# Kernel tuning notes

Hardware: AMD Instinct MI355X
Metric: run time of the kernel (lower is better)

## Reference

```python
import jax, jax.numpy as jnp
import numpy as np
from jax import lax

K = 100
NUM_CLASSES = 80
MIN_X = 1; MIN_Y = 1; MAX_X = 4; MAX_Y = 4   # int(base_layer_range/16) for [16,64,16,64]
KEEP = 300
IOU_TH = 0.5
ROI_H = 2 * MAX_Y + 1  # 9
ROI_W = 2 * MAX_X + 1  # 9
MASK_OUT = 36          # 9 -> two stride-2 deconvs -> 36
SCALE = (36.0 - 1.0) / (9.0 - 1.0)
BN_INV = 1.0 / np.sqrt(1.0 + 1e-3)  # BN eval, running mean 0 / var 1, eps=1e-3
SIZES = [(64, 64), (32, 32), (16, 16)]


def bilinear(img, xx, yy):
    # img [..., H, W]; xx, yy same shape S; border-clamped bilinear sample -> [..., *S]
    H, W = img.shape[-2], img.shape[-1]
    xx = jnp.clip(xx, 0.0, W - 1.0)
    yy = jnp.clip(yy, 0.0, H - 1.0)
    x0f = jnp.floor(xx); y0f = jnp.floor(yy)
    wx = xx - x0f; wy = yy - y0f
    x0 = x0f.astype(jnp.int32); y0 = y0f.astype(jnp.int32)
    x1 = jnp.minimum(x0 + 1, W - 1); y1 = jnp.minimum(y0 + 1, H - 1)
    v00 = img[..., y0, x0]; v01 = img[..., y0, x1]
    v10 = img[..., y1, x0]; v11 = img[..., y1, x1]
    return (1 - wy) * ((1 - wx) * v00 + wx * v01) + wy * ((1 - wx) * v10 + wx * v11)


def roi_align(feat, boxes):
    # feat [C,H,W], boxes [N,4] in feat coords -> [N,C,ROI_H,ROI_W] (sampling_ratio=1)
    n = boxes.shape[0]
    x1, y1, x2, y2 = boxes[:, 0], boxes[:, 1], boxes[:, 2], boxes[:, 3]
    jx = (jnp.arange(ROI_W, dtype=jnp.float32) + 0.5) / ROI_W
    jy = (jnp.arange(ROI_H, dtype=jnp.float32) + 0.5) / ROI_H
    gx = x1[:, None] + (x2 - x1)[:, None] * jx  # [N,ROI_W]
    gy = y1[:, None] + (y2 - y1)[:, None] * jy  # [N,ROI_H]
    xx = jnp.broadcast_to(gx[:, None, :], (n, ROI_H, ROI_W))
    yy = jnp.broadcast_to(gy[:, :, None], (n, ROI_H, ROI_W))
    out = bilinear(feat, xx, yy)  # [C,N,ROI_H,ROI_W]
    return jnp.transpose(out, (1, 0, 2, 3))


def crop_resize(masks, boxes):
    # masks [N,h,w], boxes [N,4] -> [N,MASK_OUT,MASK_OUT]
    n = boxes.shape[0]
    t = jnp.arange(MASK_OUT, dtype=jnp.float32) / (MASK_OUT - 1.0)
    x1, y1, x2, y2 = boxes[:, 0], boxes[:, 1], boxes[:, 2], boxes[:, 3]
    gx = x1[:, None] + (x2 - x1)[:, None] * t
    gy = y1[:, None] + (y2 - y1)[:, None] * t
    xx = jnp.broadcast_to(gx[:, None, :], (n, MASK_OUT, MASK_OUT))
    yy = jnp.broadcast_to(gy[:, :, None], (n, MASK_OUT, MASK_OUT))
    return jax.vmap(bilinear)(masks, xx, yy)


def nms_keep(boxes, scores):
    # greedy NMS, faithful to torchvision semantics; returns bool keep flags [N]
    n = boxes.shape[0]
    x1, y1, x2, y2 = boxes[:, 0], boxes[:, 1], boxes[:, 2], boxes[:, 3]
    area = (x2 - x1) * (y2 - y1)
    ix1 = jnp.maximum(x1[:, None], x1[None, :]); iy1 = jnp.maximum(y1[:, None], y1[None, :])
    ix2 = jnp.minimum(x2[:, None], x2[None, :]); iy2 = jnp.minimum(y2[:, None], y2[None, :])
    inter = jnp.clip(ix2 - ix1, 0.0) * jnp.clip(iy2 - iy1, 0.0)
    iou = inter / (area[:, None] + area[None, :] - inter + 1e-9)
    order = jnp.argsort(-scores)  # stable
    def step(carry, idx):
        supp, keep = carry
        k = jnp.logical_not(supp[idx])
        keep = keep.at[idx].set(k)
        supp = jnp.logical_or(supp, jnp.logical_and(k, iou[idx] > IOU_TH))
        return (supp, keep), None
    init = (jnp.zeros((n,), bool), jnp.zeros((n,), bool))
    (_, keep), _ = lax.scan(step, init, order)
    return keep


def _conv(x, w, b, pad):
    y = lax.conv_general_dilated(x, w, (1, 1), [(pad, pad), (pad, pad)],
                                 dimension_numbers=('NCHW', 'OIHW', 'NCHW'))
    return y + b[None, :, None, None]


def _deconv(x, w, b):
    # ConvTranspose2d(k=2, s=2): fractionally-strided conv, doubles spatial size
    y = lax.conv_general_dilated(x, w, (1, 1), [(1, 1), (1, 1)], lhs_dilation=(2, 2),
                                 dimension_numbers=('NCHW', 'OIHW', 'NCHW'))
    return y + b[None, :, None, None]


def _bn(x, g, b):
    return x * (g * BN_INV)[None, :, None, None] + b[None, :, None, None]


def mask_head(x, c1_w, c1_b, mid_w, mid_b, bn_g, bn_b, d1_w, d1_b, d2_w, d2_b, c5_w, c5_b, c6_w, c6_b):
    r = jax.nn.relu
    h = r(_bn(_conv(x, c1_w, c1_b, 1), bn_g[0], bn_b[0]))
    for j in range(3):  # conv2..conv4
        h = r(_bn(_conv(h, mid_w[j], mid_b[j], 1), bn_g[1 + j], bn_b[1 + j]))
    h = r(_deconv(h, d1_w, d1_b))
    h = r(_bn(_conv(h, c5_w, c5_b, 1), bn_g[4], bn_b[4]))
    h = r(_deconv(h, d2_w, d2_b))
    return jax.nn.sigmoid(_conv(h, c6_w, c6_b, 0))


def _decode_layer(heat, tlr, brr, i, H0, W0):
    C, H, W = heat.shape
    hw = H * W
    scores, inds = lax.top_k(heat.reshape(-1), K)
    clses = (inds // hw).astype(jnp.float32)
    rem = inds % hw
    ys = (rem // W).astype(jnp.float32)
    xs = (rem % W).astype(jnp.float32)
    t = tlr.reshape(2, hw)[:, rem]  # [2,K]
    b = brr.reshape(2, hw)[:, rem]
    rx = float(MAX_X - MIN_X); ry = float(MAX_Y - MIN_Y)
    cx = (MAX_X + MIN_X) / 2.0;  cy = (MAX_Y + MIN_Y) / 2.0
    tlx = jnp.clip(xs - (rx * t[0] + cx), 0.0, float(W))
    tly = jnp.clip(ys - (ry * t[1] + cy), 0.0, float(H))
    brx = jnp.clip(xs + (rx * b[0] + cx), 0.0, float(W))
    bry = jnp.clip(ys + (ry * b[1] + cy), 0.0, float(H))
    boxes = jnp.stack([tlx, tly, brx, bry], 1)
    sc = jnp.where((brx < tlx) | (bry < tly), -1.0, scores)
    mb = jnp.stack([xs - MAX_X, ys - MAX_Y, xs + MAX_X, ys + MAX_Y,
                    jnp.full((K,), float(i))], 1)
    s2, order = lax.top_k(sc, K)  # num_dets(1000) >= K -> full sort by score
    boxes = boxes[order]; mb = mb[order]; cls = clses[order]
    lay = jnp.full((K,), float(i))
    cols = jnp.stack([s2, s2, lay, cls], 1)
    bws = jnp.concatenate([boxes, cols], 1)  # boxes_without_scaling [K,8]
    scale = jnp.array([W0 / W, H0 / H, W0 / W, H0 / H], jnp.float32)
    dets = jnp.concatenate([boxes * scale, cols], 1)
    return dets, bws, mb


def _decode_one(h0, h1, h2, t0, t1, t2, b0, b1, b2, f0, f1, f2,
                c1_w, c1_b, mid_w, mid_b, bn_g, bn_b, d1_w, d1_b, d2_w, d2_b,
                c5_w, c5_b, c6_w, c6_b):
    heats = (h0, h1, h2); tls = (t0, t1, t2); brs = (b0, b1, b2); feats = (f0, f1, f2)
    H0, W0 = heats[0].shape[1], heats[0].shape[2]
    dets_l, bws_l, mb_l = [], [], []
    for i in range(3):
        d, bw, mb = _decode_layer(heats[i], tls[i], brs[i], i, H0, W0)
        dets_l.append(d); bws_l.append(bw); mb_l.append(mb)
    dets = jnp.concatenate(dets_l, 0)   # [300,8]
    bws = jnp.concatenate(bws_l, 0)
    mb = jnp.concatenate(mb_l, 0)       # [300,5]
    # NMS faithful to source: boxes = detections[:,1:5], scores = detections[:,4]
    keep = nms_keep(dets[:, 1:5], dets[:, 4])
    sel = jnp.argsort(-jnp.where(keep, dets[:, 4], -1e9))[:KEEP]
    dets = dets[sel]; bws = bws[sel]; mb = mb[sel]
    # sort by mask layer index descending (features processed last->first)
    ord2 = jnp.argsort(-mb[:, 4])
    dets = dets[ord2]; bws = bws[ord2]; mb = mb[ord2]
    # ROI pool each box from its own layer's feature map
    pooled = jnp.stack([roi_align(feats[i], mb[:, :4]) for i in range(3)], 0)  # [3,N,C,9,9]
    lay = jnp.clip(mb[:, 4].astype(jnp.int32), 0, 2)
    rois = pooled[lay, jnp.arange(KEEP)]  # [N,256,9,9]
    masks_all = mask_head(rois, c1_w, c1_b, mid_w, mid_b, bn_g, bn_b,
                          d1_w, d1_b, d2_w, d2_b, c5_w, c5_b, c6_w, c6_b)  # [N,80,36,36]
    cls = jnp.clip(dets[:, 7].astype(jnp.int32), 0, NUM_CLASSES - 1)
    masks = masks_all[jnp.arange(KEEP), cls]  # [N,36,36] (one-hot scatter/select)
    bws4 = bws[:, :4] - jnp.tile(mb[:, :2], (1, 2))
    norm_boxes = SCALE * bws4
    masks = crop_resize(masks, norm_boxes)
    return dets, masks


def setup_inputs():
    key = jax.random.key(0)
    ks = jax.random.split(key, 32)
    B = 1
    inp = {}
    for i, (H, W) in enumerate(SIZES):
        inp['heat%d' % i] = jax.random.uniform(ks[i], (B, NUM_CLASSES, H, W), jnp.float32)
        inp['tl%d' % i] = 0.1 * jax.random.normal(ks[3 + i], (B, 2, H, W), jnp.float32)
        inp['br%d' % i] = 0.1 * jax.random.normal(ks[6 + i], (B, 2, H, W), jnp.float32)
        inp['feat%d' % i] = jax.random.normal(ks[9 + i], (B, 256, H, W), jnp.float32)
    inp['c1_w'] = 0.05 * jax.random.normal(ks[12], (256, 256, 3, 3), jnp.float32)
    inp['c1_b'] = jnp.zeros((256,), jnp.float32)
    inp['mid_w'] = 0.05 * jax.random.normal(ks[13], (3, 256, 256, 3, 3), jnp.float32)
    inp['mid_b'] = jnp.zeros((3, 256), jnp.float32)
    inp['bn_g'] = jnp.ones((5, 256), jnp.float32)
    inp['bn_b'] = jnp.zeros((5, 256), jnp.float32)
    inp['d1_w'] = 0.05 * jax.random.normal(ks[14], (256, 256, 2, 2), jnp.float32)
    inp['d1_b'] = jnp.zeros((256,), jnp.float32)
    inp['d2_w'] = 0.05 * jax.random.normal(ks[15], (256, 256, 2, 2), jnp.float32)
    inp['d2_b'] = jnp.zeros((256,), jnp.float32)
    inp['c5_w'] = 0.05 * jax.random.normal(ks[16], (256, 256, 3, 3), jnp.float32)
    inp['c5_b'] = jnp.zeros((256,), jnp.float32)
    inp['c6_w'] = 0.05 * jax.random.normal(ks[17], (NUM_CLASSES, 256, 1, 1), jnp.float32)
    inp['c6_b'] = jnp.zeros((NUM_CLASSES,), jnp.float32)
    return inp


def reference(heat0, heat1, heat2, tl0, tl1, tl2, br0, br1, br2, feat0, feat1, feat2,
              c1_w, c1_b, mid_w, mid_b, bn_g, bn_b, d1_w, d1_b, d2_w, d2_b,
              c5_w, c5_b, c6_w, c6_b):
    dets, masks = jax.vmap(_decode_one, in_axes=(0,) * 12 + (None,) * 14)(
        heat0, heat1, heat2, tl0, tl1, tl2, br0, br1, br2, feat0, feat1, feat2,
        c1_w, c1_b, mid_w, mid_b, bn_g, bn_b, d1_w, d1_b, d2_w, d2_b, c5_w, c5_b, c6_w, c6_b)
    return dets, masks  # [B,300,8], [B,300,36,36]
```

## Files before the change

### kernel.cpp

```cpp
#include <hip/hip_runtime.h>
#include <math.h>

typedef __attribute__((ext_vector_type(8))) short bf16x8;
typedef __attribute__((ext_vector_type(4))) float f32x4;

__device__ __forceinline__ unsigned fkey_u(float v){
  unsigned b = __float_as_uint(v);
  return (b & 0x80000000u) ? ~b : (b | 0x80000000u);
}
__device__ __forceinline__ float fkey_inv(unsigned m){
  unsigned b = (m & 0x80000000u) ? (m & 0x7fffffffu) : ~m;
  return __uint_as_float(b);
}
__device__ __forceinline__ unsigned short f2bf(float f){
  unsigned u = __float_as_uint(f);
  unsigned r = (u + 0x7fffu + ((u>>16)&1u)) >> 16;
  return (unsigned short)r;
}
__device__ __forceinline__ unsigned long long shfl_xor_u64(unsigned long long v, int mask){
  int lo = __shfl_xor((int)(unsigned)(v & 0xFFFFFFFFull), mask, 64);
  int hi = __shfl_xor((int)(unsigned)(v >> 32), mask, 64);
  return ((unsigned long long)(unsigned)hi << 32) | (unsigned long long)(unsigned)lo;
}
#define BNI 0.9995003746877732f

template<int E, int J>
__device__ __forceinline__ void reg_step(unsigned long long* key, int t, int k2){
  #pragma unroll
  for (int r=0;r<E;r++){
    if ((r & J)==0){
      int e = t*E + r;
      bool desc = ((e & k2)==0);
      unsigned long long a=key[r], b=key[r^J];
      if (desc ? (a<b) : (a>b)){ key[r]=b; key[r^J]=a; }
    }
  }
}
template<int E>
__device__ __forceinline__ void reg_tail(unsigned long long* key, int t, int k2, int jstart){
  if constexpr (E>=8) { if (jstart>=4) reg_step<E,4>(key,t,k2); }
  if constexpr (E>=4) { if (jstart>=2) reg_step<E,2>(key,t,k2); }
  if (jstart>=1) reg_step<E,1>(key,t,k2);
}
template<int E>
__device__ void bitonic_desc(unsigned long long* key, unsigned long long* lds){
  const int t = threadIdx.x;
  const int N = E*256;
  for (int k2=2;k2<=N;k2<<=1){
    for (int j=k2>>1; j>=E; j>>=1){
      int w = j/E;
      bool lower = ((t & w)==0);
      bool desc  = (((t*E) & k2)==0);
      bool keep_max = (desc == lower);
      if (w < 64){
        #pragma unroll
        for (int r=0;r<E;r++){
          unsigned long long mine=key[r];
          unsigned long long o=shfl_xor_u64(mine, w);
          bool gt = mine > o;
          key[r] = keep_max ? (gt?mine:o) : (gt?o:mine);
        }
      } else {
        __syncthreads();
        #pragma unroll
        for (int r=0;r<E;r++) lds[t*E+r]=key[r];
        __syncthreads();
        #pragma unroll
        for (int r=0;r<E;r++){
          unsigned long long mine=key[r];
          unsigned long long o=lds[(t*E+r)^j];
          bool gt = mine > o;
          key[r] = keep_max ? (gt?mine:o) : (gt?o:mine);
        }
      }
// ... 59 lines not shown
  float Wf = (float)W;
  const float* tl = (layer==0)?tl0:((layer==1)?tl1:tl2);
  const float* br = (layer==0)?br0:((layer==1)?br1:br2);
  int base = (layer==0)?0:((layer==1)?1600:2000);
  int cnt  = (layer==0)?1600:((layer==1)?400:100);
  __shared__ unsigned long long lds[2048];
  __shared__ float scl[100];
  unsigned long long key[8];
  int t = threadIdx.x;
  #pragma unroll
  for (int r=0;r<8;r++){
    int i=t*8+r;
    key[r] = (i<cnt)? c2[base+i] : 0ull;
  }
  bitonic_desc<8>(key, lds);
  unsigned long long kwin=0;
  if (t<100) kwin = lds[t];
  float tlx=0,tly=0,brx=0,bry=0,xs=0,ys=0,clsfv=0,scv=0;
  if (t<100){
    unsigned m=(unsigned)(kwin>>32);
    unsigned gidx = 0xFFFFFFFFu - (unsigned)(kwin & 0xFFFFFFFFull);
    float val = fkey_inv(m);
    int cls = (int)(gidx / (unsigned)hw);
    int rem = (int)(gidx % (unsigned)hw);
    int iy = rem / W, ix = rem % W;
    xs = (float)ix; ys = (float)iy; clsfv = (float)cls;
    float t0=tl[rem], t1=tl[hw+rem], b0=br[rem], b1=br[hw+rem];
    tlx = fminf(fmaxf(xs - (3.0f*t0 + 2.5f), 0.0f), Wf);
    tly = fminf(fmaxf(ys - (3.0f*t1 + 2.5f), 0.0f), Wf);
    brx = fminf(fmaxf(xs + (3.0f*b0 + 2.5f), 0.0f), Wf);
    bry = fminf(fmaxf(ys + (3.0f*b1 + 2.5f), 0.0f), Wf);
    scv = ((brx<tlx)||(bry<tly)) ? -1.0f : val;
    scl[t]=scv;
  }
  __syncthreads();
  if (t<100){
    int rank=0;
    for (int i=0;i<100;i++){
      float si=scl[i];
      rank += ((si>scv)||(si==scv && i<t)) ? 1 : 0;
    }
    int row = layer*100 + rank;
    float sx = (float)(1<<layer);
    float* dr = dets + row*8;
    dr[0]=tlx*sx; dr[1]=tly*sx; dr[2]=brx*sx; dr[3]=bry*sx;
    dr[4]=scv; dr[5]=scv; dr[6]=(float)layer; dr[7]=clsfv;
    float* bwr = bws + row*8;
    bwr[0]=tlx;bwr[1]=tly;bwr[2]=brx;bwr[3]=bry;bwr[4]=scv;bwr[5]=scv;bwr[6]=(float)layer;bwr[7]=clsfv;
    float* mr = mbw + row*5;
    mr[0]=xs-4.0f; mr[1]=ys-4.0f; mr[2]=xs+4.0f; mr[3]=ys+4.0f; mr[4]=(float)layer;
  }
}

__global__ __launch_bounds__(512) void k_nms(
    const float* __restrict__ dets, const float* __restrict__ bws, const float* __restrict__ mbw,
    float* __restrict__ out_dets, float* __restrict__ mbf, int* __restrict__ clsf,
    int* __restrict__ layf, float* __restrict__ nbox)
{
  __shared__ float bx1[300],by1[300],bx2[300],by2[300],ar[300],sc[300],ly[300],kk[300],lq[300];
  __shared__ unsigned long long sm[300][5];
  __shared__ int order_[300], keep_[300], sel_[300], fperm[300];
  __shared__ unsigned long long sw[5];
  int t = threadIdx.x;
  if (t<300){
    const float* r = dets + t*8;
    bx1[t]=r[1]; by1[t]=r[2]; bx2[t]=r[3]; by2[t]=r[4];
    sc[t]=r[4];
    ar[t]=(r[3]-r[1])*(r[4]-r[2]);
    ly[t]=mbw[t*5+4];
  }
  __syncthreads();
  if (t<300){
    unsigned long long w[5]={0,0,0,0,0};
    float a=ar[t], X1=bx1[t],Y1=by1[t],X2=bx2[t],Y2=by2[t];
    for (int j=0;j<300;j++){
      float ix1=fmaxf(X1,bx1[j]), iy1=fmaxf(Y1,by1[j]);
      float ix2=fminf(X2,bx2[j]), iy2=fminf(Y2,by2[j]);
      float it = fmaxf(ix2-ix1,0.0f)*fmaxf(iy2-iy1,0.0f);
      float iou = it/(a+ar[j]-it+1e-9f);
      if (iou>0.5f) w[j>>6] |= (1ull<<(j&63));
    }
    #pragma unroll
    for (int q=0;q<5;q++) sm[t][q]=w[q];
    int rank=0; float s=sc[t];
    for (int j=0;j<300;j++){
      float sj=sc[j];
      rank += ((sj>s)||(sj==s&&j<t)) ? 1 : 0;
    }
    order_[rank]=t;
  }
  __syncthreads();
  if (t==0){
    for (int q=0;q<5;q++) sw[q]=0;
    for (int q=0;q<300;q++){
      int idx=order_[q];
      int k = (int)(!((sw[idx>>6]>>(idx&63))&1ull));
      keep_[idx]=k;
      if (k){
        for (int w2=0;w2<5;w2++) sw[w2]|=sm[idx][w2];
      }
    }
  }
  __syncthreads();
  if (t<300) kk[t] = keep_[t] ? sc[t] : -1000000000.0f;
  __syncthreads();
  if (t<300){
    float s=kk[t]; int rank=0;
    for (int j=0;j<300;j++){
      float sj=kk[j];
      rank += ((sj>s)||(sj==s&&j<t)) ? 1 : 0;
    }
    sel_[rank]=t;
  }
  __syncthreads();
  if (t<300) lq[t]=ly[sel_[t]];
  __syncthreads();
  if (t<300){
    float l=lq[t]; int rank=0;
    for (int j=0;j<300;j++){
      float lj=lq[j];
      rank += ((lj>l)||(lj==l&&j<t)) ? 1 : 0;
    }
    fperm[rank]=sel_[t];
  }
  __syncthreads();
  if (t<300){
    int src=fperm[t];
    const float* dr=dets+src*8;
    #pragma unroll
    for (int c=0;c<8;c++) out_dets[t*8+c]=dr[c];
    const float* mr=mbw+src*5;
    #pragma unroll
    for (int c=0;c<5;c++) mbf[t*5+c]=mr[c];
    int cc=(int)dr[7]; cc = cc<0?0:(cc>79?79:cc); clsf[t]=cc;
    int lv=(int)mr[4]; lv = lv<0?0:(lv>2?2:lv); layf[t]=lv;
    const float* bw=bws+src*8;
    nbox[t*4+0]=4.375f*(bw[0]-mr[0]);
    nbox[t*4+1]=4.375f*(bw[1]-mr[1]);
    nbox[t*4+2]=4.375f*(bw[2]-mr[0]);
    nbox[t*4+3]=4.375f*(bw[3]-mr[1]);
  }
}

__global__ __launch_bounds__(256) void k_roi(
    const float* __restrict__ f0,const float* __restrict__ f1,const float* __restrict__ f2,
    const float* __restrict__ mbf, const int* __restrict__ layf,
    unsigned short* __restrict__ rois, int r0)
{
  int nl = blockIdx.x; int g = r0 + nl;
  __shared__ int ix0[9], ix1[9], iy0[9], iy1[9];
  __shared__ float wx[9], wy[9];
  int lay = layf[g];
  int W = 64>>lay;
  float Wf1 = (float)(W-1);
  const float* feat = (lay==0)?f0:((lay==1)?f1:f2);
  int t=threadIdx.x;
  if (t<9){
    float x1=mbf[g*5+0], x2=mbf[g*5+2];
    float jx = ((float)t + 0.5f)/9.0f;
    float gx = x1 + (x2-x1)*jx;
    float xx = fminf(fmaxf(gx,0.0f), Wf1);
    float x0f = floorf(xx);
    wx[t]=xx-x0f;
    int x0=(int)x0f; ix0[t]=x0; ix1[t]=min(x0+1,W-1);
  } else if (t>=16 && t<25){
    int j=t-16;
    float y1=mbf[g*5+1], y2=mbf[g*5+3];
    float jy=((float)j+0.5f)/9.0f;
    float gy=y1+(y2-y1)*jy;
    float yy=fminf(fmaxf(gy,0.0f),Wf1);
    float y0f=floorf(yy);
    wy[j]=yy-y0f;
    int y0=(int)y0f; iy0[j]=y0; iy1[j]=min(y0+1,W-1);
  }
  __syncthreads();
  int c=t;
  const float* fp = feat + (size_t)c*W*W;
  unsigned short* op = rois + (size_t)nl*81*256;
  for (int p=0;p<81;p++){
    int py=p/9, px=p%9;
    float v00=fp[iy0[py]*W+ix0[px]];
    float v01=fp[iy0[py]*W+ix1[px]];
    float v10=fp[iy1[py]*W+ix0[px]];
    float v11=fp[iy1[py]*W+ix1[px]];
    float wxx=wx[px], wyy=wy[py];
    float v = (1.0f-wyy)*((1.0f-wxx)*v00 + wxx*v01) + wyy*((1.0f-wxx)*v10 + wxx*v11);
    op[(size_t)p*256 + c] = f2bf(v);
  }
}

__global__ __launch_bounds__(64) void k_wprep3(
    const float* __restrict__ c1w, const float* __restrict__ midw, const float* __restrict__ c5w,
    unsigned short* __restrict__ WB)
{
  int b = blockIdx.x, c = blockIdx.y, l = threadIdx.x;
  int t = b>>7;
  const float* src = (c==0)? c1w : (c<=3 ? midw + (size_t)(c-1)*589824 : c5w);
  unsigned short* dst = WB + (size_t)c*589824 + ((size_t)b<<9) + l*8;
  int co = (b&15)*16 + (l&15);
  int cib = ((b>>4)&7)*32 + ((l>>4)<<3);
  #pragma unroll
  for (int j=0;j<8;j++) dst[j] = f2bf(src[((size_t)co*256 + cib + j)*9 + t]);
}
__global__ __launch_bounds__(64) void k_wprep2(
    const float* __restrict__ d1w, const float* __restrict__ d2w,
    unsigned short* __restrict__ WD)
{
  int b = blockIdx.x, c = blockIdx.y, l = threadIdx.x;
  int t = b>>7;
  const float* src = (c==0)? d1w : d2w;
  unsigned short* dst = WD + (size_t)c*262144 + ((size_t)b<<9) + l*8;
  int co = (b&15)*16 + (l&15);
  int cib = ((b>>4)&7)*32 + ((l>>4)<<3);
  #pragma unroll
  for (int j=0;j<8;j++) dst[j] = f2bf(src[((size_t)co*256 + cib + j)*4 + t]);
}

__global__ __launch_bounds__(256,2) void k_mconv9(
    const unsigned short* __restrict__ Xg, unsigned short* __restrict__ Yg,
    const unsigned short* __restrict__ WBc,
    const float* __restrict__ Bc, const float* __restrict__ Gg, const float* __restrict__ Bn)
{
  __shared__ __align__(16) unsigned short Xp[121*264];
  int tid=threadIdx.x, l=tid&63, w=tid>>6;
  const unsigned short* Xr = Xg + (size_t)blockIdx.x*81*256;
  for (int idx=tid; idx<121*32; idx+=256){
    int pp=idx>>5, k8=idx&31;
    int py=pp/11-1, px=pp%11-1;
    uint4 v{0,0,0,0};
    if ((unsigned)py<9u && (unsigned)px<9u) v = *(const uint4*)(Xr + ((py*9+px)<<8) + (k8<<3));
    *(uint4*)&Xp[pp*264 + (k8<<3)] = v;
  }
  __syncthreads();
  int pixb[6];
  #pragma unroll
  for (int mt=0;mt<6;mt++){ int m=mt*16+(l&15); if(m>80)m=80; pixb[mt]=(m/9)*11+(m%9); }
  int kg=(l>>4)<<3;
  f32x4 acc[6][4] = {};
  const unsigned short* wbase = WBc + (size_t)l*8;
  for (int t9=0;t9<9;t9++){
    int toff=(t9/3)*11 + (t9%3);
    for (int kc=0;kc<8;kc++){
      bf16x8 a[6], b[4];
      #pragma unroll
      for (int mt=0;mt<6;mt++) a[mt] = *(const bf16x8*)&Xp[(pixb[mt]+toff)*264 + (kc<<5) + kg];
      #pragma unroll
      for (int nn=0;nn<4;nn++) b[nn] = *(const bf16x8*)(wbase + ((size_t)(((t9<<3)+kc)*16 + (w<<2)+nn)<<9));
      #pragma unroll
      for (int mt=0;mt<6;mt++){
        #pragma unroll
        for (int nn=0;nn<4;nn++)
          acc[mt][nn] = __builtin_amdgcn_mfma_f32_16x16x32_bf16(a[mt], b[nn], acc[mt][nn], 0,0,0);
      }
    }
  }
  unsigned short* Yr = Yg + (size_t)blockIdx.x*81*256;
  int rb=(l>>4)<<2;
  #pragma unroll
  for (int nn=0;nn<4;nn++){
    int co=(w<<6)+(nn<<4)+(l&15);
    float bc=Bc[co], gm=Gg[co]*BNI, bb=Bn[co];
    #pragma unroll
    for (int mt=0;mt<6;mt++){
      #pragma unroll
      for (int r=0;r<4;r++){
        int m=mt*16+rb+r;
        if (m<81){
          float v=fmaxf((acc[mt][nn][r]+bc)*gm+bb, 0.f);
          Yr[m*256+co]=f2bf(v);
        }
      }
    }
  }
}

__global__ __launch_bounds__(256,2) void k_mdeconv1(
    const unsigned short* __restrict__ Xg, unsigned short* __restrict__ Yg,
    const unsigned short* __restrict__ WD1, const float* __restrict__ Bd)
{
  __shared__ __align__(16) unsigned short Xp[81*264];
  int tid=threadIdx.x, l=tid&63, w=tid>>6;
  int tp=blockIdx.y;
  const unsigned short* Xr = Xg + (size_t)blockIdx.x*81*256;
  for (int idx=tid; idx<81*32; idx+=256){
    int pp=idx>>5, k8=idx&31;
    *(uint4*)&Xp[pp*264+(k8<<3)] = *(const uint4*)(Xr + (pp<<8)+(k8<<3));
  }
  __syncthreads();
  int pixb[6];
  #pragma unroll
  for (int mt=0;mt<6;mt++){ int m=mt*16+(l&15); pixb[mt]=(m>80)?80:m; }
  int kg=(l>>4)<<3;
  f32x4 acc[6][4] = {};
  const unsigned short* wbase = WD1 + (size_t)tp*65536 + (size_t)l*8;
  for (int kc=0;kc<8;kc++){
    bf16x8 a[6], b[4];
    #pragma unroll
    for (int mt=0;mt<6;mt++) a[mt] = *(const bf16x8*)&Xp[pixb[mt]*264 + (kc<<5) + kg];
    #pragma unroll
    for (int nn=0;nn<4;nn++) b[nn] = *(const bf16x8*)(wbase + ((size_t)(kc*16 + (w<<2)+nn)<<9));
    #pragma unroll
    for (int mt=0;mt<6;mt++){
      #pragma unroll
      for (int nn=0;nn<4;nn++)
        acc[mt][nn] = __builtin_amdgcn_mfma_f32_16x16x32_bf16(a[mt], b[nn], acc[mt][nn], 0,0,0);
    }
  }
  unsigned short* Yr = Yg + (size_t)blockIdx.x*324*256;
  int ky=tp>>1, kx=tp&1;
  int rb=(l>>4)<<2;
  #pragma unroll
  for (int nn=0;nn<4;nn++){
    int co=(w<<6)+(nn<<4)+(l&15);
    float bd=Bd[co];
    #pragma unroll
    for (int mt=0;mt<6;mt++){
      #pragma unroll
      for (int r=0;r<4;r++){
        int m=mt*16+rb+r;
        if (m<81){
          int iy=m/9, ix=m%9;
          int opx=(2*iy+1-ky)*18 + (2*ix+1-kx);
          Yr[opx*256+co]=f2bf(fmaxf(acc[mt][nn][r]+bd,0.f));
        }
      }
    }
  }
}

__global__ __launch_bounds__(256,2) void k_mconv18(
    const unsigned short* __restrict__ Xg, unsigned short* __restrict__ Yg,
    const unsigned short* __restrict__ WBc,
    const float* __restrict__ Bc, const float* __restrict__ Gg, const float* __restrict__ Bn)
{
  __shared__ __align__(16) unsigned short Xp[160*136];
  int tid=threadIdx.x, l=tid&63, w=tid>>6;
  int rg=blockIdx.y;
  const unsigned short* Xr = Xg + (size_t)blockIdx.x*324*256;
  int pixb[7];
  #pragma unroll
  for (int mt=0;mt<7;mt++){ int m=mt*16+(l&15); if(m>107)m=107; pixb[mt]=(m/18)*20+(m%18); }
  int kg=(l>>4)<<3;
  f32x4 acc[7][4] = {};
  const unsigned short* wbase = WBc + (size_t)l*8;
  for (int h=0;h<2;h++){
    __syncthreads();
    for (int idx=tid; idx<160*16; idx+=256){
      int pp=idx>>4, k8=idx&15;
      int py=rg*6-1+pp/20, px=pp%20-1;
      uint4 v{0,0,0,0};
      if ((unsigned)py<18u && (unsigned)px<18u)
        v = *(const uint4*)(Xr + ((py*18+px)<<8) + (h<<7) + (k8<<3));
      *(uint4*)&Xp[pp*136 + (k8<<3)] = v;
    }
    __syncthreads();
    for (int t9=0;t9<9;t9++){
      int toff=(t9/3)*20 + (t9%3);
      for (int kc=0;kc<4;kc++){
        int kcg=(h<<2)+kc;
        bf16x8 a[7], b[4];
        #pragma unroll
        for (int mt=0;mt<7;mt++) a[mt] = *(const bf16x8*)&Xp[(pixb[mt]+toff)*136 + (kc<<5) + kg];
        #pragma unroll
        for (int nn=0;nn<4;nn++) b[nn] = *(const bf16x8*)(wbase + ((size_t)(((t9<<3)+kcg)*16 + (w<<2)+nn)<<9));
        #pragma unroll
        for (int mt=0;mt<7;mt++){
          #pragma unroll
          for (int nn=0;nn<4;nn++)
            acc[mt][nn] = __builtin_amdgcn_mfma_f32_16x16x32_bf16(a[mt], b[nn], acc[mt][nn], 0,0,0);
        }
      }
    }
  }
  unsigned short* Yr = Yg + (size_t)blockIdx.x*324*256;
  int rb=(l>>4)<<2;
  #pragma unroll
  for (int nn=0;nn<4;nn++){
    int co=(w<<6)+(nn<<4)+(l&15);
    float bc=Bc[co], gm=Gg[co]*BNI, bb=Bn[co];
    #pragma unroll
    for (int mt=0;mt<7;mt++){
      #pragma unroll
      for (int r=0;r<4;r++){
        int m=mt*16+rb+r;
        if (m<108){
          int opx=rg*108+m;
          Yr[opx*256+co]=f2bf(fmaxf((acc[mt][nn][r]+bc)*gm+bb, 0.f));
        }
      }
    }
  }
}

__global__ __launch_bounds__(256,2) void k_mdec2c6(
    const unsigned short* __restrict__ Xg,
    const unsigned short* __restrict__ WD2, const float* __restrict__ Bd,
    const float* __restrict__ W6, const float* __restrict__ B6,
    const int* __restrict__ clsf, float* __restrict__ mask36, int r0)
{
  __shared__ __align__(16) unsigned short Xp[108*264];
  __shared__ float part[4][112];
  int tid=threadIdx.x, l=tid&63, w=tid>>6;
  int tp=blockIdx.y, rg=blockIdx.z;
  int g=r0+blockIdx.x;
  const unsigned short* Xr = Xg + (size_t)blockIdx.x*324*256 + (size_t)rg*108*256;
  for (int idx=tid; idx<108*32; idx+=256){
    int pp=idx>>5, k8=idx&31;
    *(uint4*)&Xp[pp*264+(k8<<3)] = *(const uint4*)(Xr + (pp<<8)+(k8<<3));
  }
  __syncthreads();
  int pixb[7];
  #pragma unroll
  for (int mt=0;mt<7;mt++){ int m=mt*16+(l&15); pixb[mt]=(m>107)?107:m; }
  int kg=(l>>4)<<3;
  f32x4 acc[7][4] = {};
  const unsigned short* wbase = WD2 + (size_t)tp*65536 + (size_t)l*8;
  for (int kc=0;kc<8;kc++){
    bf16x8 a[7], b[4];
    #pragma unroll
    for (int mt=0;mt<7;mt++) a[mt] = *(const bf16x8*)&Xp[pixb[mt]*264 + (kc<<5) + kg];
    #pragma unroll
    for (int nn=0;nn<4;nn++) b[nn] = *(const bf16x8*)(wbase + ((size_t)(kc*16 + (w<<2)+nn)<<9));
    #pragma unroll
    for (int mt=0;mt<7;mt++){
      #pragma unroll
      for (int nn=0;nn<4;nn++)
        acc[mt][nn] = __builtin_amdgcn_mfma_f32_16x16x32_bf16(a[mt], b[nn], acc[mt][nn], 0,0,0);
    }
  }
  int cls=clsf[g];
  float w6v[4], bdv[4];
// ... 66 lines not shown
  if (n_in >= 12 && in_sizes[1] == 2*64*64) {
    for (int l=0;l<3;l++){ iH[l]=l*4+0; iT[l]=l*4+1; iB[l]=l*4+2; iF[l]=l*4+3; }
  } else {
    for (int l=0;l<3;l++){ iH[l]=l; iT[l]=3+l; iB[l]=6+l; iF[l]=9+l; }
  }
  const float* heat0=(const float*)d_in[iH[0]];
  const float* heat1=(const float*)d_in[iH[1]];
  const float* heat2=(const float*)d_in[iH[2]];
  const float* tl0=(const float*)d_in[iT[0]];
  const float* tl1=(const float*)d_in[iT[1]];
  const float* tl2=(const float*)d_in[iT[2]];
  const float* br0=(const float*)d_in[iB[0]];
  const float* br1=(const float*)d_in[iB[1]];
  const float* br2=(const float*)d_in[iB[2]];
  const float* feat0=(const float*)d_in[iF[0]];
  const float* feat1=(const float*)d_in[iF[1]];
  const float* feat2=(const float*)d_in[iF[2]];
  const float* c1w=(const float*)d_in[12];
  const float* c1b=(const float*)d_in[13];
  const float* midw=(const float*)d_in[14];
  const float* midb=(const float*)d_in[15];
  const float* bng=(const float*)d_in[16];
  const float* bnb=(const float*)d_in[17];
  const float* d1w=(const float*)d_in[18];
  const float* d1b=(const float*)d_in[19];
  const float* d2w=(const float*)d_in[20];
  const float* d2b=(const float*)d_in[21];
  const float* c5w=(const float*)d_in[22];
  const float* c5b=(const float*)d_in[23];
  const float* c6w=(const float*)d_in[24];
  const float* c6b=(const float*)d_in[25];
  float* out=(float*)d_out;

  char* ws=(char*)d_ws;
  size_t cur=0;
  auto alloc=[&](size_t bytes)->char*{
    char* p=ws+cur;
    cur=(cur+bytes+255)&~(size_t)255;
    return p;
  };
  unsigned short* WB=(unsigned short*)alloc(5ull*589824*2);
  unsigned short* WD=(unsigned short*)alloc(2ull*262144*2);
  unsigned long long* c1s=(unsigned long long*)alloc(420ull*100*8);
  unsigned long long* c2s=(unsigned long long*)alloc(21ull*100*8);
  float* detsw=(float*)alloc(300*8*4);
  float* bwsw=(float*)alloc(300*8*4);
  float* mbw=(float*)alloc(300*5*4);
  float* mbf=(float*)alloc(300*5*4);
  int* clsf=(int*)alloc(300*4);
  int* layf=(int*)alloc(300*4);
  float* nbox=(float*)alloc(300*4*4);
  float* mask36=(float*)alloc(300ull*1296*4);
  size_t fixed=cur;
  size_t perroi = (size_t)(3*81 + 2*324)*256*2;
  size_t avail = (ws_size>fixed+4096)? (ws_size-fixed-4096):0;
  int NRC = (int)(avail/perroi);
  if (NRC>300) NRC=300;
  if (NRC<1) NRC=1;
  unsigned short* X0 =(unsigned short*)alloc((size_t)NRC*81*256*2);
  unsigned short* A9 =(unsigned short*)alloc((size_t)NRC*81*256*2);
  unsigned short* B9 =(unsigned short*)alloc((size_t)NRC*81*256*2);
  unsigned short* C18=(unsigned short*)alloc((size_t)NRC*324*256*2);
  unsigned short* D18=(unsigned short*)alloc((size_t)NRC*324*256*2);

  k_wprep3<<<dim3(1152,5),dim3(64),0,stream>>>(c1w,midw,c5w,WB);
  k_wprep2<<<dim3(512,2),dim3(64),0,stream>>>(d1w,d2w,WD);

  k_sel1<<<dim3(420),dim3(256),0,stream>>>(heat0,heat1,heat2,c1s);
  k_sel2<<<dim3(21),dim3(256),0,stream>>>(c1s,c2s);
  k_sel3_decode<<<dim3(3),dim3(256),0,stream>>>(c2s,tl0,tl1,tl2,br0,br1,br2,detsw,bwsw,mbw);
  k_nms<<<dim3(1),dim3(512),0,stream>>>(detsw,bwsw,mbw,out,mbf,clsf,layf,nbox);

  for (int r0=0;r0<300;r0+=NRC){
    int nr = (300-r0 < NRC)? (300-r0) : NRC;
    k_roi<<<dim3(nr),dim3(256),0,stream>>>(feat0,feat1,feat2,mbf,layf,X0,r0);
    k_mconv9<<<dim3(nr),dim3(256),0,stream>>>(X0,A9,WB,               c1b,       bng,      bnb);
    k_mconv9<<<dim3(nr),dim3(256),0,stream>>>(A9,B9,WB+1ull*589824,   midb,      bng+256,  bnb+256);
    k_mconv9<<<dim3(nr),dim3(256),0,stream>>>(B9,A9,WB+2ull*589824,   midb+256,  bng+512,  bnb+512);
    k_mconv9<<<dim3(nr),dim3(256),0,stream>>>(A9,B9,WB+3ull*589824,   midb+512,  bng+768,  bnb+768);
    k_mdeconv1<<<dim3(nr,4),dim3(256),0,stream>>>(B9,C18,WD,d1b);
    k_mconv18<<<dim3(nr,3),dim3(256),0,stream>>>(C18,D18,WB+4ull*589824, c5b, bng+1024, bnb+1024);
    k_mdec2c6<<<dim3(nr,4,3),dim3(256),0,stream>>>(D18,WD+262144,d2b,c6w,c6b,clsf,mask36,r0);
  }
  k_crop<<<dim3(300),dim3(256),0,stream>>>(mask36,nbox,out+2400);
}
```

Baseline: 693.1 us.

## Fuse ROI align with four 3x3 convs; parallelize NMS; split conv18 output channels

Result: slower. 769.6 us (+11.0%).

```diff
diff --git a/kernel.cpp b/kernel.cpp
--- a/kernel.cpp
+++ b/kernel.cpp
@@ -20,6 +20,11 @@
 __device__ __forceinline__ unsigned long long shfl_xor_u64(unsigned long long v, int mask){
   int lo = __shfl_xor((int)(unsigned)(v & 0xFFFFFFFFull), mask, 64);
   int hi = __shfl_xor((int)(unsigned)(v >> 32), mask, 64);
+  return ((unsigned long long)(unsigned)hi << 32) | (unsigned long long)(unsigned)lo;
+}
+__device__ __forceinline__ unsigned long long bshfl_u64(unsigned long long v, int lane){
+  int lo = __shfl((int)(unsigned)(v & 0xFFFFFFFFull), lane, 64);
+  int hi = __shfl((int)(unsigned)(v >> 32), lane, 64);
   return ((unsigned long long)(unsigned)hi << 32) | (unsigned long long)(unsigned)lo;
 }
 #define BNI 0.9995003746877732f
@@ -185,76 +190,122 @@
   }
 }
 
-__global__ __launch_bounds__(512) void k_nms(
+#define NMS_STEP(P, OC, M) { \
+  int idx=__shfl((OC),(P),64); \
+  unsigned long long supw=bshfl_u64(sup, idx>>6); \
+  int kq=(int)((~(supw>>(idx&63)))&1ull); \
+  if (t==0) keep_[idx]=kq; \
+  unsigned long long v0=bshfl_u64(M[0],(P)); \
+  unsigned long long v1=bshfl_u64(M[1],(P)); \
+  unsigned long long v2=bshfl_u64(M[2],(P)); \
+  unsigned long long v3=bshfl_u64(M[3],(P)); \
+  unsigned long long v4=bshfl_u64(M[4],(P)); \
+  unsigned long long mv=(t==0)?v0:((t==1)?v1:((t==2)?v2:((t==3)?v3:((t==4)?v4:0ull)))); \
+  if (kq) sup|=mv; }
+
+__global__ __launch_bounds__(320) void k_nms(
     const float* __restrict__ dets, const float* __restrict__ bws, const float* __restrict__ mbw,
     float* __restrict__ out_dets, float* __restrict__ mbf, int* __restrict__ clsf,
     int* __restrict__ layf, float* __restrict__ nbox)
 {
-  __shared__ float bx1[300],by1[300],bx2[300],by2[300],ar[300],sc[300],ly[300],kk[300],lq[300];
-  __shared__ unsigned long long sm[300][5];
+  __shared__ __align__(16) float4 bq[300];
+  __shared__ __align__(16) float sc[300];
+  __shared__ __align__(16) float kk[300];
+  __shared__ __align__(16) float lq[300];
+  __shared__ float lyv[300];
+  __shared__ unsigned long long sm_ord[300][5];
   __shared__ int order_[300], keep_[300], sel_[300], fperm[300];
-  __shared__ unsigned long long sw[5];
   int t = threadIdx.x;
+  float X1=0,Y1=0,X2=0,Y2=0,S=0,A=0;
   if (t<300){
     const float* r = dets + t*8;
-    bx1[t]=r[1]; by1[t]=r[2]; bx2[t]=r[3]; by2[t]=r[4];
-    sc[t]=r[4];
-    ar[t]=(r[3]-r[1])*(r[4]-r[2]);
-    ly[t]=mbw[t*5+4];
+    X1=r[1];Y1=r[2];X2=r[3];Y2=r[4];
+    S=r[4];
+    A=(X2-X1)*(Y2-Y1);
+    bq[t]=make_float4(X1,Y1,X2,Y2);
+    sc[t]=S;
+    lyv[t]=mbw[t*5+4];
   }
   __syncthreads();
   if (t<300){
-    unsigned long long w[5]={0,0,0,0,0};
-    float a=ar[t], X1=bx1[t],Y1=by1[t],X2=bx2[t],Y2=by2[t];
-    for (int j=0;j<300;j++){
-      float ix1=fmaxf(X1,bx1[j]), iy1=fmaxf(Y1,by1[j]);
-      float ix2=fminf(X2,bx2[j]), iy2=fminf(Y2,by2[j]);
-      float it = fmaxf(ix2-ix1,0.0f)*fmaxf(iy2-iy1,0.0f);
-      float iou = it/(a+ar[j]-it+1e-9f);
-      if (iou>0.5f) w[j>>6] |= (1ull<<(j&63));
-    }
-    #pragma unroll
-    for (int q=0;q<5;q++) sm[t][q]=w[q];
-    int rank=0; float s=sc[t];
-    for (int j=0;j<300;j++){
-      float sj=sc[j];
-      rank += ((sj>s)||(sj==s&&j<t)) ? 1 : 0;
+    int rank=0;
+    for (int j4=0;j4<75;j4++){
+      float4 s4=*(const float4*)&sc[j4*4];
+      int j=j4*4;
+      rank += ((s4.x>S)||(s4.x==S&&(j+0)<t)) ? 1:0;
+      rank += ((s4.y>S)||(s4.y==S&&(j+1)<t)) ? 1:0;
+      rank += ((s4.z>S)||(s4.z==S&&(j+2)<t)) ? 1:0;
+      rank += ((s4.w>S)||(s4.w==S&&(j+3)<t)) ? 1:0;
+    }
+    unsigned long long wrow[5];
+    #pragma unroll
+    for (int jw=0;jw<5;jw++){
+      unsigned long long bits=0;
+      int lim=(jw==4)?44:64;
+      for (int jj=0;jj<lim;jj++){
+        int j=jw*64+jj;
+        float4 q=bq[j];
+        float aj=(q.z-q.x)*(q.w-q.y);
+        float ix1=fmaxf(X1,q.x), iy1=fmaxf(Y1,q.y);
+        float ix2=fminf(X2,q.z), iy2=fminf(Y2,q.w);
+        float it=fmaxf(ix2-ix1,0.f)*fmaxf(iy2-iy1,0.f);
+        float iou=it/(A+aj-it+1e-9f);
+        bits |= ((unsigned long long)(iou>0.5f))<<jj;
+      }
+      wrow[jw]=bits;
     }
     order_[rank]=t;
-  }
-  __syncthreads();
-  if (t==0){
-    for (int q=0;q<5;q++) sw[q]=0;
-    for (int q=0;q<300;q++){
-      int idx=order_[q];
-      int k = (int)(!((sw[idx>>6]>>(idx&63))&1ull));
-      keep_[idx]=k;
-      if (k){
-        for (int w2=0;w2<5;w2++) sw[w2]|=sm[idx][w2];
-      }
-    }
+    #pragma unroll
+    for (int q=0;q<5;q++) sm_ord[rank][q]=wrow[q];
+  }
+  __syncthreads();
+  if (t<64){
+    int o0=order_[t], o1=order_[64+t], o2=order_[128+t], o3=order_[192+t];
+    int o4=(t<44)? order_[256+t] : 0;
+    unsigned long long m0[5],m1[5],m2[5],m3[5],m4[5];
+    #pragma unroll
+    for (int q=0;q<5;q++){
+      m0[q]=sm_ord[t][q]; m1[q]=sm_ord[64+t][q];
+      m2[q]=sm_ord[128+t][q]; m3[q]=sm_ord[192+t][q];
+      m4[q]=(t<44)? sm_ord[256+t][q] : 0ull;
+    }
+    unsigned long long sup=0;
+    for (int p=0;p<64;p++) NMS_STEP(p,o0,m0);
+    for (int p=0;p<64;p++) NMS_STEP(p,o1,m1);
+    for (int p=0;p<64;p++) NMS_STEP(p,o2,m2);
+    for (int p=0;p<64;p++) NMS_STEP(p,o3,m3);
+    for (int p=0;p<44;p++) NMS_STEP(p,o4,m4);
   }
   __syncthreads();
   if (t<300) kk[t] = keep_[t] ? sc[t] : -1000000000.0f;
   __syncthreads();
+  float KV=0; int rank2=0;
   if (t<300){
-    float s=kk[t]; int rank=0;
-    for (int j=0;j<300;j++){
-      float sj=kk[j];
-      rank += ((sj>s)||(sj==s&&j<t)) ? 1 : 0;
-    }
-    sel_[rank]=t;
-  }
-  __syncthreads();
-  if (t<300) lq[t]=ly[sel_[t]];
+    KV=kk[t];
+    for (int j4=0;j4<75;j4++){
+      float4 s4=*(const float4*)&kk[j4*4];
+      int j=j4*4;
+      rank2 += ((s4.x>KV)||(s4.x==KV&&(j+0)<t)) ? 1:0;
+      rank2 += ((s4.y>KV)||(s4.y==KV&&(j+1)<t)) ? 1:0;
+      rank2 += ((s4.z>KV)||(s4.z==KV&&(j+2)<t)) ? 1:0;
+      rank2 += ((s4.w>KV)||(s4.w==KV&&(j+3)<t)) ? 1:0;
+    }
+    sel_[rank2]=t;
+  }
+  __syncthreads();
+  if (t<300) lq[t]=lyv[sel_[t]];
   __syncthreads();
   if (t<300){
-    float l=lq[t]; int rank=0;
-    for (int j=0;j<300;j++){
-      float lj=lq[j];
-      rank += ((lj>l)||(lj==l&&j<t)) ? 1 : 0;
-    }
-    fperm[rank]=sel_[t];
+    float L=lq[t]; int rank3=0;
+    for (int j4=0;j4<75;j4++){
+      float4 s4=*(const float4*)&lq[j4*4];
+      int j=j4*4;
+      rank3 += ((s4.x>L)||(s4.x==L&&(j+0)<t)) ? 1:0;
+      rank3 += ((s4.y>L)||(s4.y==L&&(j+1)<t)) ? 1:0;
+      rank3 += ((s4.z>L)||(s4.z==L&&(j+2)<t)) ? 1:0;
+      rank3 += ((s4.w>L)||(s4.w==L&&(j+3)<t)) ? 1:0;
+    }
+    fperm[rank3]=sel_[t];
   }
   __syncthreads();
   if (t<300){
@@ -275,53 +326,6 @@
   }
 }
 
-__global__ __launch_bounds__(256) void k_roi(
-    const float* __restrict__ f0,const float* __restrict__ f1,const float* __restrict__ f2,
-    const float* __restrict__ mbf, const int* __restrict__ layf,
-    unsigned short* __restrict__ rois, int r0)
-{
-  int nl = blockIdx.x; int g = r0 + nl;
-  __shared__ int ix0[9], ix1[9], iy0[9], iy1[9];
-  __shared__ float wx[9], wy[9];
-  int lay = layf[g];
-  int W = 64>>lay;
-  float Wf1 = (float)(W-1);
-  const float* feat = (lay==0)?f0:((lay==1)?f1:f2);
-  int t=threadIdx.x;
-  if (t<9){
-    float x1=mbf[g*5+0], x2=mbf[g*5+2];
-    float jx = ((float)t + 0.5f)/9.0f;
-    float gx = x1 + (x2-x1)*jx;
-    float xx = fminf(fmaxf(gx,0.0f), Wf1);
-    float x0f = floorf(xx);
-    wx[t]=xx-x0f;
-    int x0=(int)x0f; ix0[t]=x0; ix1[t]=min(x0+1,W-1);
-  } else if (t>=16 && t<25){
-    int j=t-16;
-    float y1=mbf[g*5+1], y2=mbf[g*5+3];
-    float jy=((float)j+0.5f)/9.0f;
-    float gy=y1+(y2-y1)*jy;
-    float yy=fminf(fmaxf(gy,0.0f),Wf1);
-    float y0f=floorf(yy);
-    wy[j]=yy-y0f;
-    int y0=(int)y0f; iy0[j]=y0; iy1[j]=min(y0+1,W-1);
-  }
-  __syncthreads();
-  int c=t;
-  const float* fp = feat + (size_t)c*W*W;
-  unsigned short* op = rois + (size_t)nl*81*256;
-  for (int p=0;p<81;p++){
-    int py=p/9, px=p%9;
-    float v00=fp[iy0[py]*W+ix0[px]];
-    float v01=fp[iy0[py]*W+ix1[px]];
-    float v10=fp[iy1[py]*W+ix0[px]];
-    float v11=fp[iy1[py]*W+ix1[px]];
-    float wxx=wx[px], wyy=wy[py];
-    float v = (1.0f-wyy)*((1.0f-wxx)*v00 + wxx*v01) + wyy*((1.0f-wxx)*v10 + wxx*v11);
-    op[(size_t)p*256 + c] = f2bf(v);
-  }
-}
-
 __global__ __launch_bounds__(64) void k_wprep3(
     const float* __restrict__ c1w, const float* __restrict__ midw, const float* __restrict__ c5w,
     unsigned short* __restrict__ WB)
@@ -349,61 +353,117 @@
   for (int j=0;j<8;j++) dst[j] = f2bf(src[((size_t)co*256 + cib + j)*4 + t]);
 }
 
-__global__ __launch_bounds__(256,2) void k_mconv9(
-    const unsigned short* __restrict__ Xg, unsigned short* __restrict__ Yg,
-    const unsigned short* __restrict__ WBc,
-    const float* __restrict__ Bc, const float* __restrict__ Gg, const float* __restrict__ Bn)
-{
-  __shared__ __align__(16) unsigned short Xp[121*264];
+__global__ __launch_bounds__(512,1) void k_mconv9x4(
+    const float* __restrict__ f0,const float* __restrict__ f1,const float* __restrict__ f2,
+    const float* __restrict__ mbf, const int* __restrict__ layf,
+    const unsigned short* __restrict__ WB,
+    const float* __restrict__ c1b, const float* __restrict__ midb,
+    const float* __restrict__ bng, const float* __restrict__ bnb,
+    unsigned short* __restrict__ B9, int r0)
+{
+  __shared__ __align__(16) unsigned short bufA[82*264];
+  __shared__ __align__(16) unsigned short bufB[82*264];
+  __shared__ int ix0[9], ix1[9], iy0[9], iy1[9];
+  __shared__ float wxs[9], wys[9];
   int tid=threadIdx.x, l=tid&63, w=tid>>6;
-  const unsigned short* Xr = Xg + (size_t)blockIdx.x*81*256;
-  for (int idx=tid; idx<121*32; idx+=256){
-    int pp=idx>>5, k8=idx&31;
-    int py=pp/11-1, px=pp%11-1;
-    uint4 v{0,0,0,0};
-    if ((unsigned)py<9u && (unsigned)px<9u) v = *(const uint4*)(Xr + ((py*9+px)<<8) + (k8<<3));
-    *(uint4*)&Xp[pp*264 + (k8<<3)] = v;
-  }
-  __syncthreads();
-  int pixb[6];
-  #pragma unroll
-  for (int mt=0;mt<6;mt++){ int m=mt*16+(l&15); if(m>80)m=80; pixb[mt]=(m/9)*11+(m%9); }
+  int g=r0+blockIdx.x;
+  int lay=layf[g];
+  int W=64>>lay;
+  float Wf1=(float)(W-1);
+  const float* feat=(lay==0)?f0:((lay==1)?f1:f2);
+  if (tid<9){
+    float x1=mbf[g*5+0], x2=mbf[g*5+2];
+    float jx=((float)tid+0.5f)/9.0f;
+    float gx=x1+(x2-x1)*jx;
+    float xx=fminf(fmaxf(gx,0.0f),Wf1);
+    float x0f=floorf(xx);
+    wxs[tid]=xx-x0f;
+    int x0=(int)x0f; ix0[tid]=x0; ix1[tid]=min(x0+1,W-1);
+  } else if (tid>=16 && tid<25){
+    int j=tid-16;
+    float y1=mbf[g*5+1], y2=mbf[g*5+3];
+    float jy=((float)j+0.5f)/9.0f;
+    float gy=y1+(y2-y1)*jy;
+    float yy=fminf(fmaxf(gy,0.0f),Wf1);
+    float y0f=floorf(yy);
+    wys[j]=yy-y0f;
+    int y0=(int)y0f; iy0[j]=y0; iy1[j]=min(y0+1,W-1);
+  }
+  if (tid<264){ bufA[81*264+tid]=0; bufB[81*264+tid]=0; }
+  __syncthreads();
+  {
+    int c=tid&255, h=tid>>8;
+    const float* fp=feat+(size_t)c*W*W;
+    int p0=h?41:0, p1=h?81:41;
+    for (int p=p0;p<p1;p++){
+      int py=p/9, px=p%9;
+      float v00=fp[iy0[py]*W+ix0[px]];
+      float v01=fp[iy0[py]*W+ix1[px]];
+      float v10=fp[iy1[py]*W+ix0[px]];
+      float v11=fp[iy1[py]*W+ix1[px]];
+      float wxx=wxs[px], wyy=wys[py];
+      float v=(1.0f-wyy)*((1.0f-wxx)*v00+wxx*v01)+wyy*((1.0f-wxx)*v10+wxx*v11);
+      bufA[p*264+c]=f2bf(v);
+    }
+  }
+  __syncthreads();
+  int ym[6], xm[6];
+  #pragma unroll
+  for (int mt=0;mt<6;mt++){
+    int m=mt*16+(l&15); if(m>80)m=80;
+    ym[mt]=m/9; xm[mt]=m%9;
+  }
   int kg=(l>>4)<<3;
-  f32x4 acc[6][4] = {};
-  const unsigned short* wbase = WBc + (size_t)l*8;
-  for (int t9=0;t9<9;t9++){
-    int toff=(t9/3)*11 + (t9%3);
-    for (int kc=0;kc<8;kc++){
-      bf16x8 a[6], b[4];
-      #pragma unroll
-      for (int mt=0;mt<6;mt++) a[mt] = *(const bf16x8*)&Xp[(pixb[mt]+toff)*264 + (kc<<5) + kg];
-      #pragma unroll
-      for (int nn=0;nn<4;nn++) b[nn] = *(const bf16x8*)(wbase + ((size_t)(((t9<<3)+kc)*16 + (w<<2)+nn)<<9));
+  int rb=(l>>4)<<2;
+  for (int L=0;L<4;L++){
+    const unsigned short* inb=(L&1)?bufB:bufA;
+    unsigned short* outb=(L&1)?bufA:bufB;
+    const unsigned short* WL=WB+(size_t)L*589824+(size_t)l*8;
+    const float* Bc=(L==0)?c1b:(midb+(size_t)(L-1)*256);
+    const float* Gm=bng+(size_t)L*256;
+    const float* Bn=bnb+(size_t)L*256;
+    f32x4 acc[6][2] = {};
+    for (int t9=0;t9<9;t9++){
+      int dy=t9/3-1, dx=t9%3-1;
+      int rowi[6];
       #pragma unroll
       for (int mt=0;mt<6;mt++){
-        #pragma unroll
-        for (int nn=0;nn<4;nn++)
-          acc[mt][nn] = __builtin_amdgcn_mfma_f32_16x16x32_bf16(a[mt], b[nn], acc[mt][nn], 0,0,0);
+        int y=ym[mt]+dy, x=xm[mt]+dx;
+        rowi[mt]=((unsigned)y<9u&&(unsigned)x<9u)?(y*9+x):81;
       }
-    }
-  }
-  unsigned short* Yr = Yg + (size_t)blockIdx.x*81*256;
-  int rb=(l>>4)<<2;
-  #pragma unroll
-  for (int nn=0;nn<4;nn++){
-    int co=(w<<6)+(nn<<4)+(l&15);
-    float bc=Bc[co], gm=Gg[co]*BNI, bb=Bn[co];
-    #pragma unroll
-    for (int mt=0;mt<6;mt++){
-      #pragma unroll
-      for (int r=0;r<4;r++){
-        int m=mt*16+rb+r;
-        if (m<81){
-          float v=fmaxf((acc[mt][nn][r]+bc)*gm+bb, 0.f);
-          Yr[m*256+co]=f2bf(v);
+      for (int kc=0;kc<8;kc++){
+        bf16x8 a[6],b[2];
+        #pragma unroll
+        for (int mt=0;mt<6;mt++) a[mt]=*(const bf16x8*)&inb[rowi[mt]*264+(kc<<5)+kg];
+        #pragma unroll
+        for (int nn=0;nn<2;nn++) b[nn]=*(const bf16x8*)(WL+((size_t)(((t9<<3)+kc)*16+(w<<1)+nn)<<9));
+        #pragma unroll
+        for (int mt=0;mt<6;mt++){
+          #pragma unroll
+          for (int nn=0;nn<2;nn++)
+            acc[mt][nn]=__builtin_amdgcn_mfma_f32_16x16x32_bf16(a[mt],b[nn],acc[mt][nn],0,0,0);
         }
       }
     }
+    #pragma unroll
+    for (int nn=0;nn<2;nn++){
+      int co=(w<<5)+(nn<<4)+(l&15);
+      float bc=Bc[co], gm=Gm[co]*BNI, bb=Bn[co];
+      #pragma unroll
+      for (int mt=0;mt<6;mt++){
+        #pragma unroll
+        for (int r=0;r<4;r++){
+          int m=mt*16+rb+r;
+          if (m<81) outb[m*264+co]=f2bf(fmaxf((acc[mt][nn][r]+bc)*gm+bb,0.f));
+        }
+      }
+    }
+    __syncthreads();
+  }
+  unsigned short* Yr=B9+(size_t)blockIdx.x*81*256;
+  for (int idx=tid; idx<81*32; idx+=512){
+    int p=idx>>5, c8=(idx&31)<<3;
+    *(uint4*)(Yr+p*256+c8)=*(const uint4*)&bufA[p*264+c8];
   }
 }
 
@@ -468,13 +528,13 @@
 {
   __shared__ __align__(16) unsigned short Xp[160*136];
   int tid=threadIdx.x, l=tid&63, w=tid>>6;
-  int rg=blockIdx.y;
+  int rg=blockIdx.y, ch=blockIdx.z;
   const unsigned short* Xr = Xg + (size_t)blockIdx.x*324*256;
   int pixb[7];
   #pragma unroll
   for (int mt=0;mt<7;mt++){ int m=mt*16+(l&15); if(m>107)m=107; pixb[mt]=(m/18)*20+(m%18); }
   int kg=(l>>4)<<3;
-  f32x4 acc[7][4] = {};
+  f32x4 acc[7][2] = {};
   const unsigned short* wbase = WBc + (size_t)l*8;
   for (int h=0;h<2;h++){
     __syncthreads();
@@ -491,15 +551,15 @@
       int toff=(t9/3)*20 + (t9%3);
       for (int kc=0;kc<4;kc++){
         int kcg=(h<<2)+kc;
-        bf16x8 a[7], b[4];
+        bf16x8 a[7], b[2];
         #pragma unroll
         for (int mt=0;mt<7;mt++) a[mt] = *(const bf16x8*)&Xp[(pixb[mt]+toff)*136 + (kc<<5) + kg];
         #pragma unroll
-        for (int nn=0;nn<4;nn++) b[nn] = *(const bf16x8*)(wbase + ((size_t)(((t9<<3)+kcg)*16 + (w<<2)+nn)<<9));
+        for (int nn=0;nn<2;nn++) b[nn] = *(const bf16x8*)(wbase + ((size_t)(((t9<<3)+kcg)*16 + (ch<<3)+(w<<1)+nn)<<9));
         #pragma unroll
         for (int mt=0;mt<7;mt++){
           #pragma unroll
-          for (int nn=0;nn<4;nn++)
+          for (int nn=0;nn<2;nn++)
             acc[mt][nn] = __builtin_amdgcn_mfma_f32_16x16x32_bf16(a[mt], b[nn], acc[mt][nn], 0,0,0);
         }
       }
@@ -508,8 +568,8 @@
   unsigned short* Yr = Yg + (size_t)blockIdx.x*324*256;
   int rb=(l>>4)<<2;
   #pragma unroll
-  for (int nn=0;nn<4;nn++){
-    int co=(w<<6)+(nn<<4)+(l&15);
+  for (int nn=0;nn<2;nn++){
+    int co=(ch<<7)+(w<<5)+(nn<<4)+(l&15);
     float bc=Bc[co], gm=Gg[co]*BNI, bb=Bn[co];
     #pragma unroll
     for (int mt=0;mt<7;mt++){
@@ -682,13 +742,11 @@
   float* nbox=(float*)alloc(300*4*4);
   float* mask36=(float*)alloc(300ull*1296*4);
   size_t fixed=cur;
-  size_t perroi = (size_t)(3*81 + 2*324)*256*2;
+  size_t perroi = (size_t)(81 + 2*324)*256*2;
   size_t avail = (ws_size>fixed+4096)? (ws_size-fixed-4096):0;
   int NRC = (int)(avail/perroi);
   if (NRC>300) NRC=300;
   if (NRC<1) NRC=1;
-  unsigned short* X0 =(unsigned short*)alloc((size_t)NRC*81*256*2);
-  unsigned short* A9 =(unsigned short*)alloc((size_t)NRC*81*256*2);
   unsigned short* B9 =(unsigned short*)alloc((size_t)NRC*81*256*2);
   unsigned short* C18=(unsigned short*)alloc((size_t)NRC*324*256*2);
   unsigned short* D18=(unsigned short*)alloc((size_t)NRC*324*256*2);
@@ -699,17 +757,13 @@
   k_sel1<<<dim3(420),dim3(256),0,stream>>>(heat0,heat1,heat2,c1s);
   k_sel2<<<dim3(21),dim3(256),0,stream>>>(c1s,c2s);
   k_sel3_decode<<<dim3(3),dim3(256),0,stream>>>(c2s,tl0,tl1,tl2,br0,br1,br2,detsw,bwsw,mbw);
-  k_nms<<<dim3(1),dim3(512),0,stream>>>(detsw,bwsw,mbw,out,mbf,clsf,layf,nbox);
+  k_nms<<<dim3(1),dim3(320),0,stream>>>(detsw,bwsw,mbw,out,mbf,clsf,layf,nbox);
 
   for (int r0=0;r0<300;r0+=NRC){
     int nr = (300-r0 < NRC)? (300-r0) : NRC;
-    k_roi<<<dim3(nr),dim3(256),0,stream>>>(feat0,feat1,feat2,mbf,layf,X0,r0);
-    k_mconv9<<<dim3(nr),dim3(256),0,stream>>>(X0,A9,WB,               c1b,       bng,      bnb);
-    k_mconv9<<<dim3(nr),dim3(256),0,stream>>>(A9,B9,WB+1ull*589824,   midb,      bng+256,  bnb+256);
-    k_mconv9<<<dim3(nr),dim3(256),0,stream>>>(B9,A9,WB+2ull*589824,   midb+256,  bng+512,  bnb+512);
-    k_mconv9<<<dim3(nr),dim3(256),0,stream>>>(A9,B9,WB+3ull*589824,   midb+512,  bng+768,  bnb+768);
+    k_mconv9x4<<<dim3(nr),dim3(512),0,stream>>>(feat0,feat1,feat2,mbf,layf,WB,c1b,midb,bng,bnb,B9,r0);
     k_mdeconv1<<<dim3(nr,4),dim3(256),0,stream>>>(B9,C18,WD,d1b);
-    k_mconv18<<<dim3(nr,3),dim3(256),0,stream>>>(C18,D18,WB+4ull*589824, c5b, bng+1024, bnb+1024);
+    k_mconv18<<<dim3(nr,3,2),dim3(256),0,stream>>>(C18,D18,WB+4ull*589824, c5b, bng+1024, bnb+1024);
     k_mdec2c6<<<dim3(nr,4,3),dim3(256),0,stream>>>(D18,WD+262144,d2b,c6w,c6b,clsf,mask36,r0);
   }
   k_crop<<<dim3(300),dim3(256),0,stream>>>(mask36,nbox,out+2400);
```
